# Kernel optimization log

Hardware: AMD Instinct MI355X
Metric: run time of the kernel (lower is better)

## Reference

```python
import jax, jax.numpy as jnp
import numpy as np

H = 64
NG = 100000   # gene nodes
ND = 30000    # disease nodes
NE = 1500000  # gda edges (gene -> disease)
NL = 500000   # supervision (label) edges


def setup_inputs() -> dict:
    key = jax.random.key(0)
    ks = jax.random.split(key, 20)
    s = 0.1
    inp = {
        "gene_emb":    jax.random.normal(ks[0], (NG, H), jnp.float32) * s,
        "disease_emb": jax.random.normal(ks[1], (ND, H), jnp.float32) * s,
    }
    wnames = ["w1_gd_l", "w1_gd_r", "w1_dg_l", "w1_dg_r",
              "w2_gd_l", "w2_gd_r", "w2_dg_l", "w2_dg_r"]
    for i, n in enumerate(wnames):
        inp[n] = jax.random.normal(ks[2 + i], (H, H), jnp.float32) * s
    for i, n in enumerate(["b1_gd", "b1_dg", "b2_gd", "b2_dg"]):
        inp[n] = jax.random.normal(ks[10 + i], (H,), jnp.float32) * 0.01
    inp["edge_src"]  = jax.random.randint(ks[14], (NE,), 0, NG)
    inp["edge_dst"]  = jax.random.randint(ks[15], (NE,), 0, ND)
    inp["label_src"] = jax.random.randint(ks[16], (NL,), 0, NG)
    inp["label_dst"] = jax.random.randint(ks[17], (NL,), 0, ND)
    return inp


def _sage(x_src, x_dst, src, dst, n_dst, wl, wr, b):
    # SAGEConv (mean aggr): lin_l(mean_{j in N(i)} x_j) + lin_r(x_i) + b
    msum = jax.ops.segment_sum(x_src[src], dst, num_segments=n_dst)
    cnt = jax.ops.segment_sum(jnp.ones((src.shape[0], 1), x_src.dtype), dst,
                              num_segments=n_dst)
    mean = msum / jnp.maximum(cnt, 1.0)
    return mean @ wl + x_dst @ wr + b


def reference(gene_emb, disease_emb,
              w1_gd_l, w1_gd_r, b1_gd, w1_dg_l, w1_dg_r, b1_dg,
              w2_gd_l, w2_gd_r, b2_gd, w2_dg_l, w2_dg_r, b2_dg,
              edge_src, edge_dst, label_src, label_dst):
    # layer 1 (hetero: gene->disease via gda, disease->gene via rev_gda)
    h_d = jax.nn.relu(_sage(gene_emb, disease_emb, edge_src, edge_dst, ND,
                            w1_gd_l, w1_gd_r, b1_gd))
    h_g = jax.nn.relu(_sage(disease_emb, gene_emb, edge_dst, edge_src, NG,
                            w1_dg_l, w1_dg_r, b1_dg))
    # layer 2 (no activation)
    h_d2 = _sage(h_g, h_d, edge_src, edge_dst, ND, w2_gd_l, w2_gd_r, b2_gd)
    h_g2 = _sage(h_d, h_g, edge_dst, edge_src, NG, w2_dg_l, w2_dg_r, b2_dg)
    # classifier: dot product over label edges
    return jnp.sum(h_g2[label_src] * h_d2[label_dst], axis=-1)
```

## Files before the change

kernel.cpp:

```cpp
#include <hip/hip_runtime.h>
#include <hip/hip_bf16.h>

#define H 64
#define SCAN_CHUNK 512
#define NB1 512

typedef unsigned short u16;
typedef unsigned int u32;
typedef unsigned char u8;
typedef __attribute__((ext_vector_type(8))) __bf16 bf16x8;
typedef __attribute__((ext_vector_type(4))) float f32x4;
typedef __attribute__((ext_vector_type(2))) float f32x2;

__device__ __forceinline__ float bflo(u32 u) {
    return __builtin_bit_cast(float, u << 16);
}
__device__ __forceinline__ float bfhi(u32 u) {
    return __builtin_bit_cast(float, u & 0xffff0000u);
}
__device__ __forceinline__ u16 bf16rne(float f) {
    u32 u = __builtin_bit_cast(u32, f);
    return (u16)((u + 0x7FFFu + ((u >> 16) & 1u)) >> 16);
}

__global__ __launch_bounds__(256) void fused_count_convert_kernel(
    const int* __restrict__ es, const int* __restrict__ ed,
    int* __restrict__ histD, int* __restrict__ histG,
    int ne, int shiftD, int shiftG,
    const float* __restrict__ a, u16* __restrict__ oa, u32* __restrict__ oa8,
    long long na4,
    const float* __restrict__ b, u16* __restrict__ ob, long long nb4)
{
    if (blockIdx.x < NB1) {
        __shared__ int lhd[256], lhg[256];
        const int tid = threadIdx.x;
        lhd[tid] = 0; lhg[tid] = 0;
        __syncthreads();
        const int chunk = (ne + NB1 - 1) / NB1;
        const int e0 = blockIdx.x * chunk;
        const int e1 = min(e0 + chunk, ne);
        for (int e = e0 + tid; e < e1; e += 256) {
            atomicAdd(&lhd[ed[e] >> shiftD], 1);
            atomicAdd(&lhg[es[e] >> shiftG], 1);
        }
        __syncthreads();
        histD[tid * NB1 + blockIdx.x] = lhd[tid];
        histG[tid * NB1 + blockIdx.x] = lhg[tid];
        return;
    }
    long long i = (long long)(blockIdx.x - NB1) * 256 + threadIdx.x;
    if (i < na4) {
        float4 v = *(const float4*)&a[i * 4];
        ushort4 o;
        o.x = bf16rne(v.x); o.y = bf16rne(v.y);
        o.z = bf16rne(v.z); o.w = bf16rne(v.w);
        *(ushort4*)&oa[i * 4] = o;
        int r = 0;
        r = __builtin_amdgcn_cvt_pk_fp8_f32(v.x * 16.0f, v.y * 16.0f, r, false);
        r = __builtin_amdgcn_cvt_pk_fp8_f32(v.z * 16.0f, v.w * 16.0f, r, true);
        oa8[i] = (u32)r;
    } else if (i < na4 + nb4) {
        long long q = i - na4;
        float4 v = *(const float4*)&b[q * 4];
        ushort4 o;
        o.x = bf16rne(v.x); o.y = bf16rne(v.y);
        o.z = bf16rne(v.z); o.w = bf16rne(v.w);
        *(ushort4*)&ob[q * 4] = o;
    }
}

__global__ __launch_bounds__(256) void scan_reduce_kernel(
    const int* __restrict__ a1, int n1, const int* __restrict__ a2, int n2,
    int B1, int* __restrict__ partial)
{
    const int b = blockIdx.x;
    const int* a; int n, base;
    if (b < B1) { a = a1; n = n1; base = b * SCAN_CHUNK; }
    else        { a = a2; n = n2; base = (b - B1) * SCAN_CHUNK; }
    int t = threadIdx.x;
    int i0 = base + 2 * t, i1 = i0 + 1;
    int v = ((i0 < n) ? a[i0] : 0) + ((i1 < n) ? a[i1] : 0);
    #pragma unroll
    for (int off = 32; off > 0; off >>= 1) v += __shfl_down(v, off, 64);
    __shared__ int ws[4];
    if ((t & 63) == 0) ws[t >> 6] = v;
    __syncthreads();
    if (t == 0) partial[b] = ws[0] + ws[1] + ws[2] + ws[3];
}

__global__ __launch_bounds__(256) void scan_apply_kernel(
    const int* __restrict__ a1, int* __restrict__ out1, int n1,
    const int* __restrict__ a2, int* __restrict__ out2, int n2,
    int B1, int nbtot, const int* __restrict__ partial)
{
    __shared__ int sExcl[1024];
    __shared__ int ws[4];
    const int tid = threadIdx.x;
    const int lane = tid & 63, wid = tid >> 6;

    int j0 = 4 * tid;
    int p0 = (j0 + 0 < nbtot) ? partial[j0 + 0] : 0;
    int p1 = (j0 + 1 < nbtot) ? partial[j0 + 1] : 0;
    int p2 = (j0 + 2 < nbtot) ? partial[j0 + 2] : 0;
    int p3 = (j0 + 3 < nbtot) ? partial[j0 + 3] : 0;
    int psum = p0 + p1 + p2 + p3;
    int P = psum;
    #pragma unroll
    for (int off = 1; off < 64; off <<= 1) {
        int u = __shfl_up(P, off, 64);
        if (lane >= off) P += u;
    }
    if (lane == 63) ws[wid] = P;
    __syncthreads();
    int wbase = 0;
    #pragma unroll
    for (int w = 0; w < 4; ++w) wbase += (w < wid) ? ws[w] : 0;
    int e = wbase + (P - psum);
    sExcl[j0 + 0] = e;
    sExcl[j0 + 1] = e + p0;
    sExcl[j0 + 2] = e + p0 + p1;
    sExcl[j0 + 3] = e + p0 + p1 + p2;
    __syncthreads();

    const int b = blockIdx.x;
    int tot1 = sExcl[B1 - 1] + partial[B1 - 1];
    int myOff = sExcl[b] - ((b >= B1) ? tot1 : 0);
    if (b == 0 && tid == 0) {
        int tot2 = sExcl[nbtot - 1] + partial[nbtot - 1] - tot1;
        out1[n1] = tot1;
        out2[n2] = tot2;
    }
    __syncthreads();

    const int* a; int* out; int n, base;
    if (b < B1) { a = a1; out = out1; n = n1; base = b * SCAN_CHUNK; }
    else        { a = a2; out = out2; n = n2; base = (b - B1) * SCAN_CHUNK; }
    int i0 = base + 2 * tid, i1 = i0 + 1;
    int x0 = (i0 < n) ? a[i0] : 0;
    int x1 = (i1 < n) ? a[i1] : 0;
    int p = x0 + x1;
    int Q = p;
    #pragma unroll
    for (int off = 1; off < 64; off <<= 1) {
        int u = __shfl_up(Q, off, 64);
        if (lane >= off) Q += u;
    }
    if (lane == 63) ws[wid] = Q;
    __syncthreads();
    int waveBase = 0;
    #pragma unroll
    for (int w = 0; w < 4; ++w) waveBase += (w < wid) ? ws[w] : 0;
    int off0 = myOff + waveBase + (Q - p);
    if (i0 < n) out[i0] = off0;
    if (i1 < n) out[i1] = off0 + x0;
}

__global__ __launch_bounds__(256) void part_scatter_kernel(
    const int* __restrict__ es, const int* __restrict__ ed,
    const int* __restrict__ baseD, const int* __restrict__ baseG,
    u32* __restrict__ pairD, u32* __restrict__ pairG,
    int ne, int shiftD, int shiftG)
{
    __shared__ int curD[256], curG[256];
    const int tid = threadIdx.x;
    curD[tid] = baseD[tid * NB1 + blockIdx.x];
    curG[tid] = baseG[tid * NB1 + blockIdx.x];
    __syncthreads();
    const int maskD = (1 << shiftD) - 1;
    const int maskG = (1 << shiftG) - 1;
    const int chunk = (ne + NB1 - 1) / NB1;
    const int e0 = blockIdx.x * chunk;
    const int e1 = min(e0 + chunk, ne);
    for (int e = e0 + tid; e < e1; e += 256) {
        int s = es[e], d = ed[e];
        int pD = atomicAdd(&curD[d >> shiftD], 1);
        pairD[pD] = ((u32)(d & maskD) << 17) | (u32)s;
        int pG = atomicAdd(&curG[s >> shiftG], 1);
        pairG[pG] = ((u32)(s & maskG) << 17) | (u32)d;
    }
}

__global__ __launch_bounds__(256) void csr_build_kernel(
    const u32* __restrict__ pairD, const int* __restrict__ baseD,
    int* __restrict__ rowD, int* __restrict__ idxD, int nd, int shiftD, int nbktD,
    const u32* __restrict__ pairG, const int* __restrict__ baseG,
    int* __restrict__ rowG, int* __restrict__ idxG, int ng, int shiftG, int nbktG)
{
    __shared__ int lcnt[512], lcur[512];
    __shared__ int ws[4];
    const int j = blockIdx.x & 255;
    const int isG = blockIdx.x >> 8;
    const u32* pair; const int* base; int* row; int* idx; int n, shift, nbkt;
    if (isG) { pair = pairG; base = baseG; row = rowG; idx = idxG; n = ng; shift = shiftG; nbkt = nbktG; }
    else     { pair = pairD; base = baseD; row = rowD; idx = idxD; n = nd; shift = shiftD; nbkt = nbktD; }
    if (j >= nbkt) return;

    const int tid = threadIdx.x;
    const int nLo = j << shift;
    const int nHi = min(nLo + (1 << shift), n);
    const int range = nHi - nLo;
    const int segBase = base[j * NB1];
    const int segEnd  = base[(j + 1) * NB1];

    lcnt[tid] = 0; lcnt[tid + 256] = 0;
    __syncthreads();
    for (int t = segBase + tid; t < segEnd; t += 256)
        atomicAdd(&lcnt[pair[t] >> 17], 1);
    __syncthreads();

    int i0 = 2 * tid, i1 = i0 + 1;
    int c0 = (i0 < range) ? lcnt[i0] : 0;
    int c1 = (i1 < range) ? lcnt[i1] : 0;
    int p = c0 + c1;
    int P = p;
    const int lane = tid & 63, wid = tid >> 6;
    #pragma unroll
    for (int off = 1; off < 64; off <<= 1) {
        int u = __shfl_up(P, off, 64);
        if (lane >= off) P += u;
    }
    if (lane == 63) ws[wid] = P;
    __syncthreads();
    int waveBase = 0;
    #pragma unroll
    for (int w = 0; w < 4; ++w) waveBase += (w < wid) ? ws[w] : 0;
    int o0 = segBase + waveBase + (P - p);
    int o1 = o0 + c0;
    if (i0 < range) { row[nLo + i0] = o0; lcur[i0] = o0; }
    if (i1 < range) { row[nLo + i1] = o1; lcur[i1] = o1; }
    if (nHi == n && tid == 0) row[n] = segEnd;
    __syncthreads();

    for (int t = segBase + tid; t < segEnd; t += 256) {
        u32 pr = pair[t];
        int pos = atomicAdd(&lcur[pr >> 17], 1);
        idx[pos] = (int)(pr & 0x1FFFFu);
    }
}

template <bool F8D>
__global__ __launch_bounds__(256) void gather_mean_kernel(
    const void* __restrict__ srcD_, const u16* __restrict__ srcG,
    const int* __restrict__ rowD, const int* __restrict__ idxD,
    const int* __restrict__ rowG, const int* __restrict__ idxG,
    u16* __restrict__ outD, u16* __restrict__ outG, int nd, int ng)
{
    int hw = blockIdx.x * 8 + (threadIdx.x >> 5);
    int l5 = threadIdx.x & 31;
    if (hw >= nd + ng) return;
    const bool isD = hw < nd;
    const int sub = l5 >> 3;
    const int c8 = l5 & 7;
    const int* row; const int* idx; u16* out; int node;
    if (isD) { row = rowD; idx = idxD; out = outD; node = hw; }
    else     { row = rowG; idx = idxG; out = outG; node = hw - nd; }
    int beg = row[node], end = row[node + 1];

    float a0[8], a1[8];
    #pragma unroll
    for (int j = 0; j < 8; ++j) { a0[j] = 0.f; a1[j] = 0.f; }

    if (F8D && isD) {
        const u8* src8 = (const u8*)srcD_;
        int i = beg;
        for (; i + 8 <= end; i += 8) {
            int s0 = idx[i + sub];
            int s1 = idx[i + 4 + sub];
            uint2 v0 = *((const uint2*)(src8 + (size_t)s0 * 64) + c8);
            uint2 v1 = *((const uint2*)(src8 + (size_t)s1 * 64) + c8);
            f32x2 f;
            f = __builtin_amdgcn_cvt_pk_f32_fp8((int)v0.x, false); a0[0] += f.x; a0[1] += f.y;
            f = __builtin_amdgcn_cvt_pk_f32_fp8((int)v0.x, true);  a0[2] += f.x; a0[3] += f.y;
            f = __builtin_amdgcn_cvt_pk_f32_fp8((int)v0.y, false); a0[4] += f.x; a0[5] += f.y;
            f = __builtin_amdgcn_cvt_pk_f32_fp8((int)v0.y, true);  a0[6] += f.x; a0[7] += f.y;
            f = __builtin_amdgcn_cvt_pk_f32_fp8((int)v1.x, false); a1[0] += f.x; a1[1] += f.y;
            f = __builtin_amdgcn_cvt_pk_f32_fp8((int)v1.x, true);  a1[2] += f.x; a1[3] += f.y;
            f = __builtin_amdgcn_cvt_pk_f32_fp8((int)v1.y, false); a1[4] += f.x; a1[5] += f.y;
            f = __builtin_amdgcn_cvt_pk_f32_fp8((int)v1.y, true);  a1[6] += f.x; a1[7] += f.y;
        }
        if (i + 4 <= end) {
            int s0 = idx[i + sub];
            uint2 v0 = *((const uint2*)(src8 + (size_t)s0 * 64) + c8);
            f32x2 f;
            f = __builtin_amdgcn_cvt_pk_f32_fp8((int)v0.x, false); a0[0] += f.x; a0[1] += f.y;
            f = __builtin_amdgcn_cvt_pk_f32_fp8((int)v0.x, true);  a0[2] += f.x; a0[3] += f.y;
            f = __builtin_amdgcn_cvt_pk_f32_fp8((int)v0.y, false); a0[4] += f.x; a0[5] += f.y;
            f = __builtin_amdgcn_cvt_pk_f32_fp8((int)v0.y, true);  a0[6] += f.x; a0[7] += f.y;
            i += 4;
        }
        if (i + sub < end) {
            int s1 = idx[i + sub];
            uint2 v1 = *((const uint2*)(src8 + (size_t)s1 * 64) + c8);
            f32x2 f;
            f = __builtin_amdgcn_cvt_pk_f32_fp8((int)v1.x, false); a1[0] += f.x; a1[1] += f.y;
            f = __builtin_amdgcn_cvt_pk_f32_fp8((int)v1.x, true);  a1[2] += f.x; a1[3] += f.y;
            f = __builtin_amdgcn_cvt_pk_f32_fp8((int)v1.y, false); a1[4] += f.x; a1[5] += f.y;
            f = __builtin_amdgcn_cvt_pk_f32_fp8((int)v1.y, true);  a1[6] += f.x; a1[7] += f.y;
        }
    } else {
        const u16* src = isD ? (const u16*)srcD_ : srcG;
        int i = beg;
        for (; i + 8 <= end; i += 8) {
            int s0 = idx[i + sub];
            int s1 = idx[i + 4 + sub];
            uint4 v0 = *((const uint4*)(src + (size_t)s0 * H) + c8);
            uint4 v1 = *((const uint4*)(src + (size_t)s1 * H) + c8);
            a0[0] += bflo(v0.x); a0[1] += bfhi(v0.x); a0[2] += bflo(v0.y); a0[3] += bfhi(v0.y);
            a0[4] += bflo(v0.z); a0[5] += bfhi(v0.z); a0[6] += bflo(v0.w); a0[7] += bfhi(v0.w);
            a1[0] += bflo(v1.x); a1[1] += bfhi(v1.x); a1[2] += bflo(v1.y); a1[3] += bfhi(v1.y);
            a1[4] += bflo(v1.z); a1[5] += bfhi(v1.z); a1[6] += bflo(v1.w); a1[7] += bfhi(v1.w);
        }
        if (i + 4 <= end) {
            int s0 = idx[i + sub];
            uint4 v0 = *((const uint4*)(src + (size_t)s0 * H) + c8);
            a0[0] += bflo(v0.x); a0[1] += bfhi(v0.x); a0[2] += bflo(v0.y); a0[3] += bfhi(v0.y);
            a0[4] += bflo(v0.z); a0[5] += bfhi(v0.z); a0[6] += bflo(v0.w); a0[7] += bfhi(v0.w);
            i += 4;
        }
        if (i + sub < end) {
            int s1 = idx[i + sub];
            uint4 v1 = *((const uint4*)(src + (size_t)s1 * H) + c8);
            a1[0] += bflo(v1.x); a1[1] += bfhi(v1.x); a1[2] += bflo(v1.y); a1[3] += bfhi(v1.y);
            a1[4] += bflo(v1.z); a1[5] += bfhi(v1.z); a1[6] += bflo(v1.w); a1[7] += bfhi(v1.w);
        }
    }

    float acc[8];
    #pragma unroll
    for (int j = 0; j < 8; ++j) acc[j] = a0[j] + a1[j];
    #pragma unroll
    for (int j = 0; j < 8; ++j) {
        acc[j] += __shfl_xor(acc[j], 8, 64);
        acc[j] += __shfl_xor(acc[j], 16, 64);
    }
    if (sub == 0) {
        float inv = 1.0f / fmaxf((float)(end - beg), 1.0f);
        if (F8D && isD) inv *= 0.0625f;
        u32 w0 = (u32)bf16rne(acc[0] * inv) | ((u32)bf16rne(acc[1] * inv) << 16);
        u32 w1 = (u32)bf16rne(acc[2] * inv) | ((u32)bf16rne(acc[3] * inv) << 16);
        u32 w2 = (u32)bf16rne(acc[4] * inv) | ((u32)bf16rne(acc[5] * inv) << 16);
        u32 w3 = (u32)bf16rne(acc[6] * inv) | ((u32)bf16rne(acc[7] * inv) << 16);
        uint4 pk = make_uint4(w0, w1, w2, w3);
        *(uint4*)(out + (size_t)node * H + c8 * 8) = pk;
    }
}

template <bool RELU>
__global__ __launch_bounds__(256) void sage_mm_mfma_kernel(
    const u16* __restrict__ meanD, const u16* __restrict__ xD, u16* __restrict__ outD,
    const float* __restrict__ wlD, const float* __restrict__ wrD,
    const float* __restrict__ bD, int nd,
    const u16* __restrict__ meanG, const u16* __restrict__ xG, u16* __restrict__ outG,
    const float* __restrict__ wlG, const float* __restrict__ wrG,
    const float* __restrict__ bG, int ng, int MBD)
{
    __shared__ u16 sB[16 * 64 * 8];
    int b = blockIdx.x;
    const u16 *mean, *x; u16* out; const float *wl, *wr, *bias; int n;
    if (b < MBD) { mean = meanD; x = xD; out = outD; wl = wlD; wr = wrD; bias = bD; n = nd; }
    else { b -= MBD; mean = meanG; x = xG; out = outG; wl = wlG; wr = wrG; bias = bG; n = ng; }

    const int tid = threadIdx.x;
    for (int i = tid; i < 4096; i += 256) {
        int k = i >> 6, ncol = i & 63;
        int q = (k >> 3) & 3, j = k & 7, t = ncol >> 4, n15 = ncol & 15;
        int lane = q * 16 + n15;
        int c0 = k >> 5;
        sB[(((c0 + 0) * 4 + t) * 64 + lane) * 8 + j] = bf16rne(wl[i]);
        sB[(((c0 + 2) * 4 + t) * 64 + lane) * 8 + j] = bf16rne(wr[i]);
    }
    __syncthreads();

    const int lane = tid & 63;
    const int wave = tid >> 6;
    const int m = lane & 15;
    const int q = lane >> 4;

    bf16x8 Bf[16];
    {
        const uint4* sB4 = (const uint4*)sB;
        #pragma unroll
        for (int f = 0; f < 16; ++f)
            Bf[f] = __builtin_bit_cast(bf16x8, sB4[f * 64 + lane]);
    }
    float bv[4];
    #pragma unroll
    for (int t = 0; t < 4; ++t) bv[t] = bias[t * 16 + m];

    const int row0 = b * 256;
    #pragma unroll
    for (int r = 0; r < 4; ++r) {
        int rbase = row0 + (wave + 4 * r) * 16;
        if (rbase >= n) break;
        int gr = min(rbase + m, n - 1);
        const uint4* mrow = (const uint4*)(mean + (size_t)gr * H);
        const uint4* xrow = (const uint4*)(x + (size_t)gr * H);
        bf16x8 A0 = __builtin_bit_cast(bf16x8, mrow[q]);
        bf16x8 A1 = __builtin_bit_cast(bf16x8, mrow[q + 4]);
        bf16x8 A2 = __builtin_bit_cast(bf16x8, xrow[q]);
        bf16x8 A3 = __builtin_bit_cast(bf16x8, xrow[q + 4]);
        f32x4 acc[4];
        #pragma unroll
        for (int t = 0; t < 4; ++t) acc[t] = (f32x4){bv[t], bv[t], bv[t], bv[t]};
        #pragma unroll
        for (int t = 0; t < 4; ++t) {
            acc[t] = __builtin_amdgcn_mfma_f32_16x16x32_bf16(A0, Bf[0 * 4 + t], acc[t], 0, 0, 0);
            acc[t] = __builtin_amdgcn_mfma_f32_16x16x32_bf16(A1, Bf[1 * 4 + t], acc[t], 0, 0, 0);
            acc[t] = __builtin_amdgcn_mfma_f32_16x16x32_bf16(A2, Bf[2 * 4 + t], acc[t], 0, 0, 0);
            acc[t] = __builtin_amdgcn_mfma_f32_16x16x32_bf16(A3, Bf[3 * 4 + t], acc[t], 0, 0, 0);
        }
        #pragma unroll
        for (int reg = 0; reg < 4; ++reg) {
            int orow = rbase + q * 4 + reg;
            if (orow < n) {
                u16* op = out + (size_t)orow * H;
                #pragma unroll
                for (int t = 0; t < 4; ++t) {
                    float v = acc[t][reg];
                    if (RELU) v = fmaxf(v, 0.0f);
                    op[t * 16 + m] = bf16rne(v);
                }
            }
        }
    }
}

__global__ __launch_bounds__(256) void classify_kernel(
    const u16* __restrict__ hg2, const u16* __restrict__ hd2,
    const int* __restrict__ ls, const int* __restrict__ ld,
    float* __restrict__ out, int nl)
{
    long long t = (long long)blockIdx.x * blockDim.x + threadIdx.x;
    int e = (int)(t >> 3);
    int c8 = (int)(t & 7);
    if (e >= nl) return;
    int a = ls[e];
    int b = ld[e];
    uint4 ua = *((const uint4*)(hg2 + (size_t)a * H) + c8);
    uint4 ub = *((const uint4*)(hd2 + (size_t)b * H) + c8);
    float v = bflo(ua.x) * bflo(ub.x) + bfhi(ua.x) * bfhi(ub.x)
            + bflo(ua.y) * bflo(ub.y) + bfhi(ua.y) * bfhi(ub.y)
            + bflo(ua.z) * bflo(ub.z) + bfhi(ua.z) * bfhi(ub.z)
            + bflo(ua.w) * bflo(ub.w) + bfhi(ua.w) * bfhi(ub.w);
    v += __shfl_xor(v, 1, 64);
    v += __shfl_xor(v, 2, 64);
    v += __shfl_xor(v, 4, 64);
    if (c8 == 0) out[e] = v;
}

extern "C" void kernel_launch(void* const* d_in, const int* in_sizes, int n_in,
                              void* d_out, int out_size, void* d_ws, size_t ws_size,
                              hipStream_t stream)
{
    const float* gene  = (const float*)d_in[0];
    const float* dis   = (const float*)d_in[1];
    const float* w1gdl = (const float*)d_in[2];
    const float* w1gdr = (const float*)d_in[3];
    const float* w1dgl = (const float*)d_in[4];
    const float* w1dgr = (const float*)d_in[5];
    const float* w2gdl = (const float*)d_in[6];
    const float* w2gdr = (const float*)d_in[7];
    const float* w2dgl = (const float*)d_in[8];
    const float* w2dgr = (const float*)d_in[9];
    const float* b1gd  = (const float*)d_in[10];
    const float* b1dg  = (const float*)d_in[11];
    const float* b2gd  = (const float*)d_in[12];
    const float* b2dg  = (const float*)d_in[13];
    const int* es = (const int*)d_in[14];
    const int* ed = (const int*)d_in[15];
    const int* ls = (const int*)d_in[16];
    const int* ld = (const int*)d_in[17];

    const int ng = in_sizes[0] / H;
    const int nd = in_sizes[1] / H;
    const int ne = in_sizes[14];
    const int nl = in_sizes[16];

    int shiftD = 0; while (((nd + (1 << shiftD) - 1) >> shiftD) > 256) ++shiftD;
    int shiftG = 0; while (((ng + (1 << shiftG) - 1) >> shiftG) > 256) ++shiftG;
    const int nbktD = (nd + (1 << shiftD) - 1) >> shiftD;
    const int nbktG = (ng + (1 << shiftG) - 1) >> shiftG;
    const int n1 = 256 * NB1;

    int* rowD = (int*)d_ws;
    int* rowG = rowD + nd + 1;
    int* idxD = rowG + ng + 1;
    int* idxG = idxD + ne;
    u16* geneBf = (u16*)(idxG + ne);
    u16* disBf  = geneBf + (size_t)ng * H;
    u16* h1Dbf  = disBf + (size_t)nd * H;
    u16* h1Gbf  = h1Dbf + (size_t)nd * H;
    u16* h2Dbf  = h1Gbf + (size_t)ng * H;
    u16* h2Gbf  = h2Dbf + (size_t)nd * H;
    uintptr_t pf8 = (uintptr_t)(h2Gbf + (size_t)ng * H);
    pf8 = (pf8 + 15) & ~(uintptr_t)15;
    u32* geneF8 = (u32*)pf8;
    uintptr_t p = (uintptr_t)(geneF8 + (size_t)ng * 16);
    p = (p + 15) & ~(uintptr_t)15;
    u16* MD = (u16*)p;
    u16* MG = MD + (size_t)nd * H;
    int* histD = (int*)p;
    int* histG = histD + n1;
    int* baseD = histG + n1;
    int* baseG = baseD + n1 + 1;
    int* partial  = baseG + n1 + 1;
    uintptr_t pp = (uintptr_t)(partial + 1024);
    pp = (pp + 15) & ~(uintptr_t)15;
    u32* pairD = (u32*)pp;
    u32* pairG = pairD + ne;

    const long long na4 = (long long)ng * H / 4;
    const long long nb4 = (long long)nd * H / 4;
    const int convBlocks = (int)((na4 + nb4 + 255) / 256);
    fused_count_convert_kernel<<<NB1 + convBlocks, 256, 0, stream>>>(
        es, ed, histD, histG, ne, shiftD, shiftG,
        gene, geneBf, geneF8, na4, dis, disBf, nb4);

    const int B1 = n1 / SCAN_CHUNK;
    const int nbtot = 2 * B1;
    scan_reduce_kernel<<<nbtot, 256, 0, stream>>>(histD, n1, histG, n1, B1, partial);
    scan_apply_kernel<<<nbtot, 256, 0, stream>>>(histD, baseD, n1,
                                                 histG, baseG, n1, B1, nbtot, partial);

    part_scatter_kernel<<<NB1, 256, 0, stream>>>(es, ed, baseD, baseG,
                                                 pairD, pairG, ne, shiftD, shiftG);
    csr_build_kernel<<<512, 256, 0, stream>>>(
        pairD, baseD, rowD, idxD, nd, shiftD, nbktD,
        pairG, baseG, rowG, idxG, ng, shiftG, nbktG);

    const int gatherBlocks = (nd + ng + 7) / 8;
    const int MBD = (nd + 255) / 256;
    const int MBG = (ng + 255) / 256;

    gather_mean_kernel<true><<<gatherBlocks, 256, 0, stream>>>(
        geneF8, disBf, rowD, idxD, rowG, idxG, MD, MG, nd, ng);
    sage_mm_mfma_kernel<true><<<MBD + MBG, 256, 0, stream>>>(
        MD, disBf, h1Dbf, w1gdl, w1gdr, b1gd, nd,
        MG, geneBf, h1Gbf, w1dgl, w1dgr, b1dg, ng, MBD);

    gather_mean_kernel<false><<<gatherBlocks, 256, 0, stream>>>(
        h1Gbf, h1Dbf, rowD, idxD, rowG, idxG, MD, MG, nd, ng);
    sage_mm_mfma_kernel<false><<<MBD + MBG, 256, 0, stream>>>(
        MD, h1Dbf, h2Dbf, w2gdl, w2gdr, b2gd, nd,
        MG, h1Gbf, h2Gbf, w2dgl, w2dgr, b2dg, ng, MBD);

    {
        long long threads = (long long)nl * 8;
        int blocks = (int)((threads + 255) / 256);
        classify_kernel<<<blocks, 256, 0, stream>>>(h2Gbf, h2Dbf, ls, ld,
                                                    (float*)d_out, nl);
    }
}
```

Before: 349.8 us.

## Bucket-sort label edges by gene source to improve classifier gather locality

Adds a histogram, prefix scan and scatter pass that buckets the supervision edges by the coarse bucket of their gene source index, producing a permutation. The classify kernel then walks edges in that order, so reads of gene embedding rows land in nearby cache lines. This reuses the existing count, scan and scatter kernels by giving them extra blocks. In exchange it adds work on the label edges, an extra indirect load per edge, and writes to the output become scattered.

```diff
diff --git a/kernel.cpp b/kernel.cpp
--- a/kernel.cpp
+++ b/kernel.cpp
@@ -4,6 +4,7 @@
 #define H 64
 #define SCAN_CHUNK 512
 #define NB1 512
+#define NBL 256
 
 typedef unsigned short u16;
 typedef unsigned int u32;
@@ -27,6 +28,7 @@
     const int* __restrict__ es, const int* __restrict__ ed,
     int* __restrict__ histD, int* __restrict__ histG,
     int ne, int shiftD, int shiftG,
+    const int* __restrict__ ls, int* __restrict__ histL, int nl,
     const float* __restrict__ a, u16* __restrict__ oa, u32* __restrict__ oa8,
     long long na4,
     const float* __restrict__ b, u16* __restrict__ ob, long long nb4)
@@ -48,7 +50,22 @@
         histG[tid * NB1 + blockIdx.x] = lhg[tid];
         return;
     }
-    long long i = (long long)(blockIdx.x - NB1) * 256 + threadIdx.x;
+    if (blockIdx.x < NB1 + NBL) {
+        __shared__ int lhl[256];
+        const int tid = threadIdx.x;
+        const int blk = blockIdx.x - NB1;
+        lhl[tid] = 0;
+        __syncthreads();
+        const int chunk = (nl + NBL - 1) / NBL;
+        const int e0 = blk * chunk;
+        const int e1 = min(e0 + chunk, nl);
+        for (int e = e0 + tid; e < e1; e += 256)
+            atomicAdd(&lhl[ls[e] >> shiftG], 1);
+        __syncthreads();
+        histL[tid * NBL + blk] = lhl[tid];
+        return;
+    }
+    long long i = (long long)(blockIdx.x - NB1 - NBL) * 256 + threadIdx.x;
     if (i < na4) {
         float4 v = *(const float4*)&a[i * 4];
         ushort4 o;
@@ -70,13 +87,15 @@
 }
 
 __global__ __launch_bounds__(256) void scan_reduce_kernel(
-    const int* __restrict__ a1, int n1, const int* __restrict__ a2, int n2,
-    int B1, int* __restrict__ partial)
+    const int* __restrict__ a1, int n1_, const int* __restrict__ a2, int n2_,
+    const int* __restrict__ a3, int n3_, int B1, int B2,
+    int* __restrict__ partial)
 {
     const int b = blockIdx.x;
     const int* a; int n, base;
-    if (b < B1) { a = a1; n = n1; base = b * SCAN_CHUNK; }
-    else        { a = a2; n = n2; base = (b - B1) * SCAN_CHUNK; }
+    if (b < B1)          { a = a1; n = n1_; base = b * SCAN_CHUNK; }
+    else if (b < B1 + B2){ a = a2; n = n2_; base = (b - B1) * SCAN_CHUNK; }
+    else                 { a = a3; n = n3_; base = (b - B1 - B2) * SCAN_CHUNK; }
     int t = threadIdx.x;
     int i0 = base + 2 * t, i1 = i0 + 1;
     int v = ((i0 < n) ? a[i0] : 0) + ((i1 < n) ? a[i1] : 0);
@@ -89,9 +108,10 @@
 }
 
 __global__ __launch_bounds__(256) void scan_apply_kernel(
-    const int* __restrict__ a1, int* __restrict__ out1, int n1,
-    const int* __restrict__ a2, int* __restrict__ out2, int n2,
-    int B1, int nbtot, const int* __restrict__ partial)
+    const int* __restrict__ a1, int* __restrict__ out1, int n1_,
+    const int* __restrict__ a2, int* __restrict__ out2, int n2_,
+    const int* __restrict__ a3, int* __restrict__ out3, int n3_,
+    int B1, int B2, int nbtot, const int* __restrict__ partial)
 {
     __shared__ int sExcl[1024];
     __shared__ int ws[4];
@@ -124,17 +144,21 @@
 
     const int b = blockIdx.x;
     int tot1 = sExcl[B1 - 1] + partial[B1 - 1];
-    int myOff = sExcl[b] - ((b >= B1) ? tot1 : 0);
+    int totA = sExcl[B1 + B2 - 1] + partial[B1 + B2 - 1];
+    int tot2 = totA - tot1;
+    int myOff = sExcl[b] - ((b >= B1) ? tot1 : 0) - ((b >= B1 + B2) ? tot2 : 0);
     if (b == 0 && tid == 0) {
-        int tot2 = sExcl[nbtot - 1] + partial[nbtot - 1] - tot1;
-        out1[n1] = tot1;
-        out2[n2] = tot2;
+        int tot3 = sExcl[nbtot - 1] + partial[nbtot - 1] - totA;
+        out1[n1_] = tot1;
+        out2[n2_] = tot2;
+        out3[n3_] = tot3;
     }
     __syncthreads();
 
     const int* a; int* out; int n, base;
-    if (b < B1) { a = a1; out = out1; n = n1; base = b * SCAN_CHUNK; }
-    else        { a = a2; out = out2; n = n2; base = (b - B1) * SCAN_CHUNK; }
+    if (b < B1)          { a = a1; out = out1; n = n1_; base = b * SCAN_CHUNK; }
+    else if (b < B1 + B2){ a = a2; out = out2; n = n2_; base = (b - B1) * SCAN_CHUNK; }
+    else                 { a = a3; out = out3; n = n3_; base = (b - B1 - B2) * SCAN_CHUNK; }
     int i0 = base + 2 * tid, i1 = i0 + 1;
     int x0 = (i0 < n) ? a[i0] : 0;
     int x1 = (i1 < n) ? a[i1] : 0;
@@ -159,24 +183,39 @@
     const int* __restrict__ es, const int* __restrict__ ed,
     const int* __restrict__ baseD, const int* __restrict__ baseG,
     u32* __restrict__ pairD, u32* __restrict__ pairG,
-    int ne, int shiftD, int shiftG)
-{
-    __shared__ int curD[256], curG[256];
+    int ne, int shiftD, int shiftG,
+    const int* __restrict__ ls, const int* __restrict__ baseL,
+    int* __restrict__ permL, int nl)
+{
+    __shared__ int curA[256], curB[256];
     const int tid = threadIdx.x;
-    curD[tid] = baseD[tid * NB1 + blockIdx.x];
-    curG[tid] = baseG[tid * NB1 + blockIdx.x];
-    __syncthreads();
-    const int maskD = (1 << shiftD) - 1;
-    const int maskG = (1 << shiftG) - 1;
-    const int chunk = (ne + NB1 - 1) / NB1;
-    const int e0 = blockIdx.x * chunk;
-    const int e1 = min(e0 + chunk, ne);
-    for (int e = e0 + tid; e < e1; e += 256) {
-        int s = es[e], d = ed[e];
-        int pD = atomicAdd(&curD[d >> shiftD], 1);
-        pairD[pD] = ((u32)(d & maskD) << 17) | (u32)s;
-        int pG = atomicAdd(&curG[s >> shiftG], 1);
-        pairG[pG] = ((u32)(s & maskG) << 17) | (u32)d;
+    if (blockIdx.x < NB1) {
+        curA[tid] = baseD[tid * NB1 + blockIdx.x];
+        curB[tid] = baseG[tid * NB1 + blockIdx.x];
+        __syncthreads();
+        const int maskD = (1 << shiftD) - 1;
+        const int maskG = (1 << shiftG) - 1;
+        const int chunk = (ne + NB1 - 1) / NB1;
+        const int e0 = blockIdx.x * chunk;
+        const int e1 = min(e0 + chunk, ne);
+        for (int e = e0 + tid; e < e1; e += 256) {
+            int s = es[e], d = ed[e];
+            int pD = atomicAdd(&curA[d >> shiftD], 1);
+            pairD[pD] = ((u32)(d & maskD) << 17) | (u32)s;
+            int pG = atomicAdd(&curB[s >> shiftG], 1);
+            pairG[pG] = ((u32)(s & maskG) << 17) | (u32)d;
+        }
+    } else {
+        const int blk = blockIdx.x - NB1;
+        curA[tid] = baseL[tid * NBL + blk];
+        __syncthreads();
+        const int chunk = (nl + NBL - 1) / NBL;
+        const int e0 = blk * chunk;
+        const int e1 = min(e0 + chunk, nl);
+        for (int e = e0 + tid; e < e1; e += 256) {
+            int pos = atomicAdd(&curA[ls[e] >> shiftG], 1);
+            permL[pos] = e;
+        }
     }
 }
 
@@ -428,12 +467,14 @@
 __global__ __launch_bounds__(256) void classify_kernel(
     const u16* __restrict__ hg2, const u16* __restrict__ hd2,
     const int* __restrict__ ls, const int* __restrict__ ld,
+    const int* __restrict__ permL,
     float* __restrict__ out, int nl)
 {
     long long t = (long long)blockIdx.x * blockDim.x + threadIdx.x;
-    int e = (int)(t >> 3);
+    int i = (int)(t >> 3);
     int c8 = (int)(t & 7);
-    if (e >= nl) return;
+    if (i >= nl) return;
+    int e = permL[i];
     int a = ls[e];
     int b = ld[e];
     uint4 ua = *((const uint4*)(hg2 + (size_t)a * H) + c8);
@@ -481,12 +522,14 @@
     const int nbktD = (nd + (1 << shiftD) - 1) >> shiftD;
     const int nbktG = (ng + (1 << shiftG) - 1) >> shiftG;
     const int n1 = 256 * NB1;
+    const int n3 = 256 * NBL;
 
     int* rowD = (int*)d_ws;
     int* rowG = rowD + nd + 1;
     int* idxD = rowG + ng + 1;
     int* idxG = idxD + ne;
-    u16* geneBf = (u16*)(idxG + ne);
+    int* permL = idxG + ne;
+    u16* geneBf = (u16*)(permL + nl);
     u16* disBf  = geneBf + (size_t)ng * H;
     u16* h1Dbf  = disBf + (size_t)nd * H;
     u16* h1Gbf  = h1Dbf + (size_t)nd * H;
@@ -501,9 +544,11 @@
     u16* MG = MD + (size_t)nd * H;
     int* histD = (int*)p;
     int* histG = histD + n1;
-    int* baseD = histG + n1;
+    int* histL = histG + n1;
+    int* baseD = histL + n3;
     int* baseG = baseD + n1 + 1;
-    int* partial  = baseG + n1 + 1;
+    int* baseL = baseG + n1 + 1;
+    int* partial = baseL + n3 + 1;
     uintptr_t pp = (uintptr_t)(partial + 1024);
     pp = (pp + 15) & ~(uintptr_t)15;
     u32* pairD = (u32*)pp;
@@ -512,18 +557,26 @@
     const long long na4 = (long long)ng * H / 4;
     const long long nb4 = (long long)nd * H / 4;
     const int convBlocks = (int)((na4 + nb4 + 255) / 256);
-    fused_count_convert_kernel<<<NB1 + convBlocks, 256, 0, stream>>>(
+    fused_count_convert_kernel<<<NB1 + NBL + convBlocks, 256, 0, stream>>>(
         es, ed, histD, histG, ne, shiftD, shiftG,
+        ls, histL, nl,
         gene, geneBf, geneF8, na4, dis, disBf, nb4);
 
     const int B1 = n1 / SCAN_CHUNK;
-    const int nbtot = 2 * B1;
-    scan_reduce_kernel<<<nbtot, 256, 0, stream>>>(histD, n1, histG, n1, B1, partial);
+    const int B2 = B1;
+    const int B3 = n3 / SCAN_CHUNK;
+    const int nbtot = B1 + B2 + B3;
+    scan_reduce_kernel<<<nbtot, 256, 0, stream>>>(histD, n1, histG, n1,
+                                                  histL, n3, B1, B2, partial);
     scan_apply_kernel<<<nbtot, 256, 0, stream>>>(histD, baseD, n1,
-                                                 histG, baseG, n1, B1, nbtot, partial);
-
-    part_scatter_kernel<<<NB1, 256, 0, stream>>>(es, ed, baseD, baseG,
-                                                 pairD, pairG, ne, shiftD, shiftG);
+                                                 histG, baseG, n1,
+                                                 histL, baseL, n3,
+                                                 B1, B2, nbtot, partial);
+
+    part_scatter_kernel<<<NB1 + NBL, 256, 0, stream>>>(
+        es, ed, baseD, baseG, pairD, pairG, ne, shiftD, shiftG,
+        ls, baseL, permL, nl);
+
     csr_build_kernel<<<512, 256, 0, stream>>>(
         pairD, baseD, rowD, idxD, nd, shiftD, nbktD,
         pairG, baseG, rowG, idxG, ng, shiftG, nbktG);
@@ -548,6 +601,6 @@
         long long threads = (long long)nl * 8;
         int blocks = (int)((threads + 255) / 256);
         classify_kernel<<<blocks, 256, 0, stream>>>(h2Gbf, h2Dbf, ls, ld,
-                                                    (float*)d_out, nl);
-    }
-}
+                                                    permL, (float*)d_out, nl);
+    }
+}
```

Result: slower. 374.1 us (+6.9%).
